# Performance work log

Measured on AMD Instinct MI355X. Metric: run time of the kernel, lower is better.

The kernel has to match this reference:

```python
import jax, jax.numpy as jnp
import numpy as np
from jax import lax

N_POINTS = 4_194_304
HIDDEN = 16
N_HIDDEN_LAYERS = 8   # num_layers=9 -> 1 input layer + 8 bias-free hidden layers


def setup_inputs() -> dict:
    key = jax.random.key(0)
    k_x, k_win, k_bin, k_wh, k_wout = jax.random.split(key, 5)
    x = jax.random.uniform(k_x, (N_POINTS, 2), dtype=jnp.float32)
    # PyTorch Linear default init: U(-1/sqrt(fan_in), 1/sqrt(fan_in))
    s_in = 1.0 / np.sqrt(2.0)
    s_h = 1.0 / np.sqrt(HIDDEN)
    W_in = jax.random.uniform(k_win, (HIDDEN, 2), jnp.float32, -s_in, s_in)
    b_in = jax.random.uniform(k_bin, (HIDDEN,), jnp.float32, -s_in, s_in)
    W_hidden = jax.random.uniform(k_wh, (N_HIDDEN_LAYERS, HIDDEN, HIDDEN), jnp.float32, -s_h, s_h)
    W_out = jax.random.uniform(k_wout, (3, HIDDEN), jnp.float32, -s_h, s_h)
    return {"x": x, "W_in": W_in, "b_in": b_in, "W_hidden": W_hidden, "W_out": W_out}


def reference(x, W_in, b_in, W_hidden, W_out):
    # [N,2] -> [N,16], biased input layer + tanh
    h = jnp.tanh(x @ W_in.T + b_in)
    # 8 bias-free 16x16 layers, each followed by tanh
    def step(h, W):
        return jnp.tanh(h @ W.T), None
    h, _ = lax.scan(step, h, W_hidden)
    # output layer 16 -> 3, sigmoid to map to [0,1] RGB
    return jax.nn.sigmoid(h @ W_out.T)
```

## Files before the change

### kernel.cpp

```cpp
#include <hip/hip_runtime.h>


typedef float  f32x4 __attribute__((ext_vector_type(4)));
typedef __fp16 f16x4 __attribute__((ext_vector_type(4)));
typedef __fp16 f16x2 __attribute__((ext_vector_type(2)));

#define K2   2.8853900817779268f
#define KOUT (-1.4426950408889634f)

__device__ __forceinline__ f16x4 v4s(f32x4 y) {
    float e0 = __builtin_amdgcn_exp2f(y[0]);
    float e1 = __builtin_amdgcn_exp2f(y[1]);
    float e2 = __builtin_amdgcn_exp2f(y[2]);
    float e3 = __builtin_amdgcn_exp2f(y[3]);
    float d0 = e0 + 1.0f, d1 = e1 + 1.0f, d2 = e2 + 1.0f, d3 = e3 + 1.0f;
    float p01 = d0 * d1, p23 = d2 * d3;
    float r   = __builtin_amdgcn_rcpf(p01 * p23);
    float i01 = r * p23, i23 = r * p01;
    float v0 = i01 * d1, v1 = i01 * d0;
    float v2 = i23 * d3, v3 = i23 * d2;
    f16x2 lo = __builtin_amdgcn_cvt_pkrtz(v0, v1);
    f16x2 hi = __builtin_amdgcn_cvt_pkrtz(v2, v3);
    return __builtin_shufflevector(lo, hi, 0, 1, 2, 3);
}

__global__ __launch_bounds__(256, 6)
void artnet_kernel(const float2* __restrict__ x,
                   const float2* __restrict__ Win,
                   const float*  __restrict__ bin,
                   const float4* __restrict__ Wh,
                   const float4* __restrict__ Wout,
                   float* __restrict__ out,
                   int nPairs, int nWaves)
{
    const int tid  = blockIdx.x * 256 + threadIdx.x;
    const int gw   = tid >> 6;
    const int lane = threadIdx.x & 63;
    const int row  = lane & 15;
    const int quad = lane >> 4;

    f16x4 aw[8];
    f32x4 crs[8];
#pragma unroll
    for (int l = 0; l < 8; ++l) {
        float4 w = Wh[l * 64 + row * 4 + quad];
        const float s = -2.0f * K2;
        f16x2 lo = __builtin_amdgcn_cvt_pkrtz(w.x * s, w.y * s);
        f16x2 hi = __builtin_amdgcn_cvt_pkrtz(w.z * s, w.w * s);
        aw[l] = __builtin_shufflevector(lo, hi, 0, 1, 2, 3);
        float partial = w.x + w.y + w.z + w.w;
        partial += __shfl_xor(partial, 16, 64);
        partial += __shfl_xor(partial, 32, 64);
        f32x4 c;
#pragma unroll
        for (int i = 0; i < 4; ++i)
            c[i] = K2 * __shfl(partial, quad * 4 + i, 64);
        crs[l] = c;
    }

    f16x4 awin = {(__fp16)0.0f, (__fp16)0.0f, (__fp16)0.0f, (__fp16)0.0f};
    if (quad == 0) {
        float2 wr = Win[row];
        f16x2 lo = __builtin_amdgcn_cvt_pkrtz(wr.x * K2, wr.y * K2);
        f16x2 hi = __builtin_amdgcn_cvt_pkrtz(bin[row] * K2, 0.0f);
        awin = __builtin_shufflevector(lo, hi, 0, 1, 2, 3);
    }

    f16x4 awo = {(__fp16)0.0f, (__fp16)0.0f, (__fp16)0.0f, (__fp16)0.0f};
    float prt = 0.0f;
    if (row < 3) {
        float4 w = Wout[row * 4 + quad];
        const float s = -2.0f * KOUT;
        f16x2 lo = __builtin_amdgcn_cvt_pkrtz(w.x * s, w.y * s);
        f16x2 hi = __builtin_amdgcn_cvt_pkrtz(w.z * s, w.w * s);
        awo = __builtin_shufflevector(lo, hi, 0, 1, 2, 3);
        prt = w.x + w.y + w.z + w.w;
    }
    prt += __shfl_xor(prt, 16, 64);
    prt += __shfl_xor(prt, 32, 64);
    f32x4 crso;
#pragma unroll
    for (int i = 0; i < 4; ++i)
        crso[i] = KOUT * __shfl(prt, quad * 4 + i, 64);

    const f32x4 zero4 = {0.0f, 0.0f, 0.0f, 0.0f};
    const f16x2 one0  = {(__fp16)1.0f, (__fp16)0.0f};

    int pi = gw;
    float2 xa, xb;
    if (pi < nPairs) {
        xa = x[pi * 32 + row];
        xb = x[pi * 32 + 16 + row];
    }

    while (pi < nPairs) {
        const int pn = pi + nWaves;
        const int t0 = pi * 2;

        f16x2 la = __builtin_amdgcn_cvt_pkrtz(xa.x, xa.y);
        f16x2 lb = __builtin_amdgcn_cvt_pkrtz(xb.x, xb.y);
        f16x4 bf0 = __builtin_shufflevector(la, one0, 0, 1, 2, 3);
        f16x4 bf1 = __builtin_shufflevector(lb, one0, 0, 1, 2, 3);

        if (pn < nPairs) {
            xa = x[pn * 32 + row];
            xb = x[pn * 32 + 16 + row];
        }

        f32x4 a0 = __builtin_amdgcn_mfma_f32_16x16x16f16(awin, bf0, zero4, 0, 0, 0);
        f32x4 a1 = __builtin_amdgcn_mfma_f32_16x16x16f16(awin, bf1, zero4, 0, 0, 0);
        bf0 = v4s(a0);
        bf1 = v4s(a1);

#pragma unroll
        for (int l = 0; l < 8; ++l) {
            f32x4 y0 = __builtin_amdgcn_mfma_f32_16x16x16f16(aw[l], bf0, crs[l], 0, 0, 0);
            f32x4 y1 = __builtin_amdgcn_mfma_f32_16x16x16f16(aw[l], bf1, crs[l], 0, 0, 0);
            bf0 = v4s(y0);
            bf1 = v4s(y1);
        }

        f32x4 acco0 = __builtin_amdgcn_mfma_f32_16x16x16f16(awo, bf0, crso, 0, 0, 0);
        f32x4 acco1 = __builtin_amdgcn_mfma_f32_16x16x16f16(awo, bf1, crso, 0, 0, 0);

        float t10 = __shfl_xor(acco1[0], 16, 64);
        float t11 = __shfl_xor(acco1[1], 16, 64);
        float t12 = __shfl_xor(acco1[2], 16, 64);
        if (quad < 2) {
            float y0 = (quad == 0) ? acco0[0] : t10;
            float y1 = (quad == 0) ? acco0[1] : t11;
            float y2 = (quad == 0) ? acco0[2] : t12;
            float d0 = __builtin_amdgcn_exp2f(y0) + 1.0f;
            float d1 = __builtin_amdgcn_exp2f(y1) + 1.0f;
            float d2 = __builtin_amdgcn_exp2f(y2) + 1.0f;
            float p01 = d0 * d1;
            float r   = __builtin_amdgcn_rcpf(p01 * d2);
            float s2  = r * p01;
            float t   = r * d2;
            float s0  = t * d1, s1 = t * d0;
            const int p = t0 * 16 + row + (quad << 4);
            float3 o;
            o.x = s0; o.y = s1; o.z = s2;
            *reinterpret_cast<float3*>(out + p * 3) = o;
        }

        pi = pn;
    }
}

extern "C" void kernel_launch(void* const* d_in, const int* in_sizes, int n_in,
                              void* d_out, int out_size, void* d_ws, size_t ws_size,
                              hipStream_t stream) {
    const float2* x    = (const float2*)d_in[0];
    const float2* Win  = (const float2*)d_in[1];
    const float*  bin  = (const float*) d_in[2];
    const float4* Wh   = (const float4*)d_in[3];
    const float4* Wout = (const float4*)d_in[4];
    float* out = (float*)d_out;

    const int n      = in_sizes[0] / 2;
    const int nPairs = n / 32;
    const int blocks = 4096;
    const int nWaves = blocks * 4;

    artnet_kernel<<<blocks, 256, 0, stream>>>(x, Win, bin, Wh, Wout, out, nPairs, nWaves);
}
```

Baseline: 191.4 us.

## Process four 16-point tiles per wave iteration and pack outputs via block-diagonal MFMA

Each wave iteration now handles four 16-point tiles instead of two, which gives more independent MFMA/transcendental chains to interleave. The per-layer bias vectors move from registers into LDS and are reloaded each layer, freeing VGPRs for the wider tiling. The output layer uses four block-diagonal weight fragments that accumulate all four tiles into a single accumulator, so every lane holds one point's RGB and the cross-lane shuffles and idle half-wave disappear. The costs are an LDS read per layer, a __syncthreads, and scalar stores in place of float3 stores.

```diff
diff --git a/kernel.cpp b/kernel.cpp
--- a/kernel.cpp
+++ b/kernel.cpp
@@ -31,7 +31,7 @@
                    const float4* __restrict__ Wh,
                    const float4* __restrict__ Wout,
                    float* __restrict__ out,
-                   int nPairs, int nWaves)
+                   int nQuads, int nWaves)
 {
     const int tid  = blockIdx.x * 256 + threadIdx.x;
     const int gw   = tid >> 6;
@@ -39,8 +39,9 @@
     const int row  = lane & 15;
     const int quad = lane >> 4;
 
+    __shared__ __align__(16) float crs_lds[8][16];
+
     f16x4 aw[8];
-    f32x4 crs[8];
 #pragma unroll
     for (int l = 0; l < 8; ++l) {
         float4 w = Wh[l * 64 + row * 4 + quad];
@@ -51,11 +52,8 @@
         float partial = w.x + w.y + w.z + w.w;
         partial += __shfl_xor(partial, 16, 64);
         partial += __shfl_xor(partial, 32, 64);
-        f32x4 c;
-#pragma unroll
-        for (int i = 0; i < 4; ++i)
-            c[i] = K2 * __shfl(partial, quad * 4 + i, 64);
-        crs[l] = c;
+        if (threadIdx.x < 16)
+            crs_lds[l][row] = K2 * partial;
     }
 
     f16x4 awin = {(__fp16)0.0f, (__fp16)0.0f, (__fp16)0.0f, (__fp16)0.0f};
@@ -66,14 +64,24 @@
         awin = __builtin_shufflevector(lo, hi, 0, 1, 2, 3);
     }
 
-    f16x4 awo = {(__fp16)0.0f, (__fp16)0.0f, (__fp16)0.0f, (__fp16)0.0f};
+    const f16x4 zf16 = {(__fp16)0.0f, (__fp16)0.0f, (__fp16)0.0f, (__fp16)0.0f};
+    f16x4 wobase = zf16;
+    const int r3 = row & 3;
+    if (r3 < 3) {
+        float4 w = Wout[r3 * 4 + quad];
+        const float s = -2.0f * KOUT;
+        f16x2 lo = __builtin_amdgcn_cvt_pkrtz(w.x * s, w.y * s);
+        f16x2 hi = __builtin_amdgcn_cvt_pkrtz(w.z * s, w.w * s);
+        wobase = __builtin_shufflevector(lo, hi, 0, 1, 2, 3);
+    }
+    f16x4 awos[4];
+#pragma unroll
+    for (int s = 0; s < 4; ++s)
+        awos[s] = ((row >> 2) == s) ? wobase : zf16;
+
     float prt = 0.0f;
     if (row < 3) {
         float4 w = Wout[row * 4 + quad];
-        const float s = -2.0f * KOUT;
-        f16x2 lo = __builtin_amdgcn_cvt_pkrtz(w.x * s, w.y * s);
-        f16x2 hi = __builtin_amdgcn_cvt_pkrtz(w.z * s, w.w * s);
-        awo = __builtin_shufflevector(lo, hi, 0, 1, 2, 3);
         prt = w.x + w.y + w.z + w.w;
     }
     prt += __shfl_xor(prt, 16, 64);
@@ -81,70 +89,75 @@
     f32x4 crso;
 #pragma unroll
     for (int i = 0; i < 4; ++i)
-        crso[i] = KOUT * __shfl(prt, quad * 4 + i, 64);
+        crso[i] = (i < 3) ? KOUT * __shfl(prt, i, 64) : 0.0f;
+
+    __syncthreads();
 
     const f32x4 zero4 = {0.0f, 0.0f, 0.0f, 0.0f};
     const f16x2 one0  = {(__fp16)1.0f, (__fp16)0.0f};
 
-    int pi = gw;
-    float2 xa, xb;
-    if (pi < nPairs) {
-        xa = x[pi * 32 + row];
-        xb = x[pi * 32 + 16 + row];
+    int qi = gw;
+    float2 xp[4];
+    if (qi < nQuads) {
+#pragma unroll
+        for (int s = 0; s < 4; ++s)
+            xp[s] = x[(qi * 4 + s) * 16 + row];
     }
 
-    while (pi < nPairs) {
-        const int pn = pi + nWaves;
-        const int t0 = pi * 2;
+    while (qi < nQuads) {
+        const int qn = qi + nWaves;
 
-        f16x2 la = __builtin_amdgcn_cvt_pkrtz(xa.x, xa.y);
-        f16x2 lb = __builtin_amdgcn_cvt_pkrtz(xb.x, xb.y);
-        f16x4 bf0 = __builtin_shufflevector(la, one0, 0, 1, 2, 3);
-        f16x4 bf1 = __builtin_shufflevector(lb, one0, 0, 1, 2, 3);
-
-        if (pn < nPairs) {
-            xa = x[pn * 32 + row];
-            xb = x[pn * 32 + 16 + row];
+        f16x4 bf[4];
+#pragma unroll
+        for (int s = 0; s < 4; ++s) {
+            f16x2 lo = __builtin_amdgcn_cvt_pkrtz(xp[s].x, xp[s].y);
+            bf[s] = __builtin_shufflevector(lo, one0, 0, 1, 2, 3);
         }
 
-        f32x4 a0 = __builtin_amdgcn_mfma_f32_16x16x16f16(awin, bf0, zero4, 0, 0, 0);
-        f32x4 a1 = __builtin_amdgcn_mfma_f32_16x16x16f16(awin, bf1, zero4, 0, 0, 0);
-        bf0 = v4s(a0);
-        bf1 = v4s(a1);
+        if (qn < nQuads) {
+#pragma unroll
+            for (int s = 0; s < 4; ++s)
+                xp[s] = x[(qn * 4 + s) * 16 + row];
+        }
+
+        f32x4 y0 = __builtin_amdgcn_mfma_f32_16x16x16f16(awin, bf[0], zero4, 0, 0, 0);
+        f32x4 y1 = __builtin_amdgcn_mfma_f32_16x16x16f16(awin, bf[1], zero4, 0, 0, 0);
+        f32x4 y2 = __builtin_amdgcn_mfma_f32_16x16x16f16(awin, bf[2], zero4, 0, 0, 0);
+        f32x4 y3 = __builtin_amdgcn_mfma_f32_16x16x16f16(awin, bf[3], zero4, 0, 0, 0);
+        bf[0] = v4s(y0); bf[1] = v4s(y1); bf[2] = v4s(y2); bf[3] = v4s(y3);
 
 #pragma unroll
         for (int l = 0; l < 8; ++l) {
-            f32x4 y0 = __builtin_amdgcn_mfma_f32_16x16x16f16(aw[l], bf0, crs[l], 0, 0, 0);
-            f32x4 y1 = __builtin_amdgcn_mfma_f32_16x16x16f16(aw[l], bf1, crs[l], 0, 0, 0);
-            bf0 = v4s(y0);
-            bf1 = v4s(y1);
+            f32x4 c = *(const f32x4*)&crs_lds[l][quad * 4];
+            f32x4 t0 = __builtin_amdgcn_mfma_f32_16x16x16f16(aw[l], bf[0], c, 0, 0, 0);
+            f32x4 t1 = __builtin_amdgcn_mfma_f32_16x16x16f16(aw[l], bf[1], c, 0, 0, 0);
+            f32x4 t2 = __builtin_amdgcn_mfma_f32_16x16x16f16(aw[l], bf[2], c, 0, 0, 0);
+            f32x4 t3 = __builtin_amdgcn_mfma_f32_16x16x16f16(aw[l], bf[3], c, 0, 0, 0);
+            bf[0] = v4s(t0); bf[1] = v4s(t1); bf[2] = v4s(t2); bf[3] = v4s(t3);
         }
 
-        f32x4 acco0 = __builtin_amdgcn_mfma_f32_16x16x16f16(awo, bf0, crso, 0, 0, 0);
-        f32x4 acco1 = __builtin_amdgcn_mfma_f32_16x16x16f16(awo, bf1, crso, 0, 0, 0);
+        f32x4 acc;
+        acc = __builtin_amdgcn_mfma_f32_16x16x16f16(awos[0], bf[0], crso, 0, 0, 0);
+        acc = __builtin_amdgcn_mfma_f32_16x16x16f16(awos[1], bf[1], acc,  0, 0, 0);
+        acc = __builtin_amdgcn_mfma_f32_16x16x16f16(awos[2], bf[2], acc,  0, 0, 0);
+        acc = __builtin_amdgcn_mfma_f32_16x16x16f16(awos[3], bf[3], acc,  0, 0, 0);
 
-        float t10 = __shfl_xor(acco1[0], 16, 64);
-        float t11 = __shfl_xor(acco1[1], 16, 64);
-        float t12 = __shfl_xor(acco1[2], 16, 64);
-        if (quad < 2) {
-            float y0 = (quad == 0) ? acco0[0] : t10;
-            float y1 = (quad == 0) ? acco0[1] : t11;
-            float y2 = (quad == 0) ? acco0[2] : t12;
-            float d0 = __builtin_amdgcn_exp2f(y0) + 1.0f;
-            float d1 = __builtin_amdgcn_exp2f(y1) + 1.0f;
-            float d2 = __builtin_amdgcn_exp2f(y2) + 1.0f;
+        {
+            float d0 = __builtin_amdgcn_exp2f(acc[0]) + 1.0f;
+            float d1 = __builtin_amdgcn_exp2f(acc[1]) + 1.0f;
+            float d2 = __builtin_amdgcn_exp2f(acc[2]) + 1.0f;
             float p01 = d0 * d1;
             float r   = __builtin_amdgcn_rcpf(p01 * d2);
             float s2  = r * p01;
             float t   = r * d2;
             float s0  = t * d1, s1 = t * d0;
-            const int p = t0 * 16 + row + (quad << 4);
-            float3 o;
-            o.x = s0; o.y = s1; o.z = s2;
-            *reinterpret_cast<float3*>(out + p * 3) = o;
+            const int p = (qi * 4 + quad) * 16 + row;
+            out[p * 3 + 0] = s0;
+            out[p * 3 + 1] = s1;
+            out[p * 3 + 2] = s2;
         }
 
-        pi = pn;
+        qi = qn;
     }
 }
 
@@ -159,9 +172,9 @@
     float* out = (float*)d_out;
 
     const int n      = in_sizes[0] / 2;
-    const int nPairs = n / 32;
+    const int nQuads = n / 64;
     const int blocks = 4096;
     const int nWaves = blocks * 4;
 
-    artnet_kernel<<<blocks, 256, 0, stream>>>(x, Win, bin, Wh, Wout, out, nPairs, nWaves);
+    artnet_kernel<<<blocks, 256, 0, stream>>>(x, Win, bin, Wh, Wout, out, nQuads, nWaves);
 }
```

New measurement: 208.6 us. 9.0% more time.

## Share one reciprocal across both tiles, move layer biases to LDS, merge output MFMAs

Applied to the files above, without the earlier changes.

The sigmoid-style activation now computes a single reciprocal for eight values spanning both point tiles instead of one per four values, which cuts transcendental work. The per-layer bias vectors move from registers to shared memory to lower register pressure, at the cost of an LDS read on every layer. The output layer packs both tiles into one accumulator using two chained MFMAs with row-masked weights, which removes the cross-lane shuffles. Products of eight (1+e) terms risk overflow to inf, and the stores become three scalar writes.

```diff
diff --git a/kernel.cpp b/kernel.cpp
--- a/kernel.cpp
+++ b/kernel.cpp
@@ -8,20 +8,34 @@
 #define K2   2.8853900817779268f
 #define KOUT (-1.4426950408889634f)
 
-__device__ __forceinline__ f16x4 v4s(f32x4 y) {
-    float e0 = __builtin_amdgcn_exp2f(y[0]);
-    float e1 = __builtin_amdgcn_exp2f(y[1]);
-    float e2 = __builtin_amdgcn_exp2f(y[2]);
-    float e3 = __builtin_amdgcn_exp2f(y[3]);
+__device__ __forceinline__ void v8s(f32x4 ya, f32x4 yb, f16x4& va, f16x4& vb) {
+    float e0 = __builtin_amdgcn_exp2f(ya[0]);
+    float e1 = __builtin_amdgcn_exp2f(ya[1]);
+    float e2 = __builtin_amdgcn_exp2f(ya[2]);
+    float e3 = __builtin_amdgcn_exp2f(ya[3]);
+    float e4 = __builtin_amdgcn_exp2f(yb[0]);
+    float e5 = __builtin_amdgcn_exp2f(yb[1]);
+    float e6 = __builtin_amdgcn_exp2f(yb[2]);
+    float e7 = __builtin_amdgcn_exp2f(yb[3]);
     float d0 = e0 + 1.0f, d1 = e1 + 1.0f, d2 = e2 + 1.0f, d3 = e3 + 1.0f;
+    float d4 = e4 + 1.0f, d5 = e5 + 1.0f, d6 = e6 + 1.0f, d7 = e7 + 1.0f;
     float p01 = d0 * d1, p23 = d2 * d3;
-    float r   = __builtin_amdgcn_rcpf(p01 * p23);
-    float i01 = r * p23, i23 = r * p01;
+    float p45 = d4 * d5, p67 = d6 * d7;
+    float q03 = p01 * p23, q47 = p45 * p67;
+    float r   = __builtin_amdgcn_rcpf(q03 * q47);
+    float rA  = r * q47, rB = r * q03;
+    float i01 = rA * p23, i23 = rA * p01;
+    float i45 = rB * p67, i67 = rB * p45;
     float v0 = i01 * d1, v1 = i01 * d0;
     float v2 = i23 * d3, v3 = i23 * d2;
-    f16x2 lo = __builtin_amdgcn_cvt_pkrtz(v0, v1);
-    f16x2 hi = __builtin_amdgcn_cvt_pkrtz(v2, v3);
-    return __builtin_shufflevector(lo, hi, 0, 1, 2, 3);
+    float v4 = i45 * d5, v5 = i45 * d4;
+    float v6 = i67 * d7, v7 = i67 * d6;
+    f16x2 la = __builtin_amdgcn_cvt_pkrtz(v0, v1);
+    f16x2 ha = __builtin_amdgcn_cvt_pkrtz(v2, v3);
+    f16x2 lb = __builtin_amdgcn_cvt_pkrtz(v4, v5);
+    f16x2 hb = __builtin_amdgcn_cvt_pkrtz(v6, v7);
+    va = __builtin_shufflevector(la, ha, 0, 1, 2, 3);
+    vb = __builtin_shufflevector(lb, hb, 0, 1, 2, 3);
 }
 
 __global__ __launch_bounds__(256, 6)
@@ -39,8 +53,9 @@
     const int row  = lane & 15;
     const int quad = lane >> 4;
 
+    __shared__ __align__(16) float crs_lds[8][16];
+
     f16x4 aw[8];
-    f32x4 crs[8];
 #pragma unroll
     for (int l = 0; l < 8; ++l) {
         float4 w = Wh[l * 64 + row * 4 + quad];
@@ -51,11 +66,8 @@
         float partial = w.x + w.y + w.z + w.w;
         partial += __shfl_xor(partial, 16, 64);
         partial += __shfl_xor(partial, 32, 64);
-        f32x4 c;
-#pragma unroll
-        for (int i = 0; i < 4; ++i)
-            c[i] = K2 * __shfl(partial, quad * 4 + i, 64);
-        crs[l] = c;
+        if (threadIdx.x < 16)
+            crs_lds[l][row] = K2 * partial;
     }
 
     f16x4 awin = {(__fp16)0.0f, (__fp16)0.0f, (__fp16)0.0f, (__fp16)0.0f};
@@ -66,14 +78,23 @@
         awin = __builtin_shufflevector(lo, hi, 0, 1, 2, 3);
     }
 
-    f16x4 awo = {(__fp16)0.0f, (__fp16)0.0f, (__fp16)0.0f, (__fp16)0.0f};
+    const f16x4 zf16 = {(__fp16)0.0f, (__fp16)0.0f, (__fp16)0.0f, (__fp16)0.0f};
+    f16x4 wobase = zf16;
+    const int r3 = row & 3;
+    if (r3 < 3) {
+        float4 w = Wout[r3 * 4 + quad];
+        const float s = -2.0f * KOUT;
+        f16x2 lo = __builtin_amdgcn_cvt_pkrtz(w.x * s, w.y * s);
+        f16x2 hi = __builtin_amdgcn_cvt_pkrtz(w.z * s, w.w * s);
+        wobase = __builtin_shufflevector(lo, hi, 0, 1, 2, 3);
+    }
+    f16x4 awos2[2];
+    awos2[0] = ((row >> 2) == 0) ? wobase : zf16;
+    awos2[1] = ((row >> 2) == 1) ? wobase : zf16;
+
     float prt = 0.0f;
     if (row < 3) {
         float4 w = Wout[row * 4 + quad];
-        const float s = -2.0f * KOUT;
-        f16x2 lo = __builtin_amdgcn_cvt_pkrtz(w.x * s, w.y * s);
-        f16x2 hi = __builtin_amdgcn_cvt_pkrtz(w.z * s, w.w * s);
-        awo = __builtin_shufflevector(lo, hi, 0, 1, 2, 3);
         prt = w.x + w.y + w.z + w.w;
     }
     prt += __shfl_xor(prt, 16, 64);
@@ -81,7 +102,9 @@
     f32x4 crso;
 #pragma unroll
     for (int i = 0; i < 4; ++i)
-        crso[i] = KOUT * __shfl(prt, quad * 4 + i, 64);
+        crso[i] = (i < 3) ? KOUT * __shfl(prt, i, 64) : 0.0f;
+
+    __syncthreads();
 
     const f32x4 zero4 = {0.0f, 0.0f, 0.0f, 0.0f};
     const f16x2 one0  = {(__fp16)1.0f, (__fp16)0.0f};
@@ -95,7 +118,6 @@
 
     while (pi < nPairs) {
         const int pn = pi + nWaves;
-        const int t0 = pi * 2;
 
         f16x2 la = __builtin_amdgcn_cvt_pkrtz(xa.x, xa.y);
         f16x2 lb = __builtin_amdgcn_cvt_pkrtz(xb.x, xb.y);
@@ -107,41 +129,35 @@
             xb = x[pn * 32 + 16 + row];
         }
 
-        f32x4 a0 = __builtin_amdgcn_mfma_f32_16x16x16f16(awin, bf0, zero4, 0, 0, 0);
-        f32x4 a1 = __builtin_amdgcn_mfma_f32_16x16x16f16(awin, bf1, zero4, 0, 0, 0);
-        bf0 = v4s(a0);
-        bf1 = v4s(a1);
+        f32x4 y0 = __builtin_amdgcn_mfma_f32_16x16x16f16(awin, bf0, zero4, 0, 0, 0);
+        f32x4 y1 = __builtin_amdgcn_mfma_f32_16x16x16f16(awin, bf1, zero4, 0, 0, 0);
+        v8s(y0, y1, bf0, bf1);
 
 #pragma unroll
         for (int l = 0; l < 8; ++l) {
-            f32x4 y0 = __builtin_amdgcn_mfma_f32_16x16x16f16(aw[l], bf0, crs[l], 0, 0, 0);
-            f32x4 y1 = __builtin_amdgcn_mfma_f32_16x16x16f16(aw[l], bf1, crs[l], 0, 0, 0);
-            bf0 = v4s(y0);
-            bf1 = v4s(y1);
+            f32x4 c = *(const f32x4*)&crs_lds[l][quad * 4];
+            f32x4 t0 = __builtin_amdgcn_mfma_f32_16x16x16f16(aw[l], bf0, c, 0, 0, 0);
+            f32x4 t1 = __builtin_amdgcn_mfma_f32_16x16x16f16(aw[l], bf1, c, 0, 0, 0);
+            v8s(t0, t1, bf0, bf1);
         }
 
-        f32x4 acco0 = __builtin_amdgcn_mfma_f32_16x16x16f16(awo, bf0, crso, 0, 0, 0);
-        f32x4 acco1 = __builtin_amdgcn_mfma_f32_16x16x16f16(awo, bf1, crso, 0, 0, 0);
+        f32x4 acc;
+        acc = __builtin_amdgcn_mfma_f32_16x16x16f16(awos2[0], bf0, crso, 0, 0, 0);
+        acc = __builtin_amdgcn_mfma_f32_16x16x16f16(awos2[1], bf1, acc,  0, 0, 0);
 
-        float t10 = __shfl_xor(acco1[0], 16, 64);
-        float t11 = __shfl_xor(acco1[1], 16, 64);
-        float t12 = __shfl_xor(acco1[2], 16, 64);
         if (quad < 2) {
-            float y0 = (quad == 0) ? acco0[0] : t10;
-            float y1 = (quad == 0) ? acco0[1] : t11;
-            float y2 = (quad == 0) ? acco0[2] : t12;
-            float d0 = __builtin_amdgcn_exp2f(y0) + 1.0f;
-            float d1 = __builtin_amdgcn_exp2f(y1) + 1.0f;
-            float d2 = __builtin_amdgcn_exp2f(y2) + 1.0f;
+            float d0 = __builtin_amdgcn_exp2f(acc[0]) + 1.0f;
+            float d1 = __builtin_amdgcn_exp2f(acc[1]) + 1.0f;
+            float d2 = __builtin_amdgcn_exp2f(acc[2]) + 1.0f;
             float p01 = d0 * d1;
             float r   = __builtin_amdgcn_rcpf(p01 * d2);
             float s2  = r * p01;
             float t   = r * d2;
             float s0  = t * d1, s1 = t * d0;
-            const int p = t0 * 16 + row + (quad << 4);
-            float3 o;
-            o.x = s0; o.y = s1; o.z = s2;
-            *reinterpret_cast<float3*>(out + p * 3) = o;
+            const int p = (pi * 2 + quad) * 16 + row;
+            out[p * 3 + 0] = s0;
+            out[p * 3 + 1] = s1;
+            out[p * 3 + 2] = s2;
         }
 
         pi = pn;
```

After: 188.0 us. About the same (-1.8%).
